# Kernel optimization log

Hardware: AMD Instinct MI355X
Metric: run time of the kernel (lower is better)

The kernel has to match this reference:

```python
import jax, jax.numpy as jnp
import numpy as np

B_, L_, D_, N_ = 2, 2048, 512, 64

def setup_inputs() -> dict:
    key = jax.random.key(0)
    ks = jax.random.split(key, 6)
    s = 1.0 / np.sqrt(D_)
    return {
        "x": jax.random.normal(ks[0], (B_, L_, D_), dtype=jnp.float32),
        "W1": jax.random.normal(ks[1], (D_, D_), dtype=jnp.float32) * s,
        "b1": jnp.zeros((D_,), dtype=jnp.float32),
        "W2": jax.random.normal(ks[2], (D_, N_), dtype=jnp.float32) * s,
        "b2": jnp.zeros((N_,), dtype=jnp.float32),
        "W3": jax.random.normal(ks[3], (D_, N_), dtype=jnp.float32) * s,
        "b3": jnp.zeros((N_,), dtype=jnp.float32),
        "A": jax.random.normal(ks[4], (D_, N_), dtype=jnp.float32) * (1.0 / np.sqrt(N_)),
    }

def reference(x, W1, b1, W2, b2, W3, b3, A):
    # Projections (faithful to fc2/fc3/fc1 in the torch module)
    B = x @ W2 + b2                                  # (b, l, n)
    C = x @ W3 + b3                                  # (b, l, n)
    delta = jax.nn.softplus(x @ W1 + b1)             # (b, l, d)
    # Discretization
    dB = jnp.einsum('bld,bln->bldn', delta, B)       # (b, l, d, n)
    dA = jnp.exp(jnp.einsum('bld,dn->bldn', delta, A))  # (b, l, d, n)
    # h is initialized to zeros in the original forward, so the dA*h term
    # contributes exactly zero; kept for faithfulness to the source math.
    h = dA * 0.0 + x[..., None] * dB                 # (b, l, d, n)
    y = jnp.einsum('bln,bldn->bld', C, h)            # (b, l, d)
    return y
```

## Files before the change

### kernel.cpp

```cpp
#include <hip/hip_runtime.h>
#include <math.h>

#define DDIM 512
#define MTOK 4096

typedef _Float16 f16;
typedef _Float16 f16x4 __attribute__((ext_vector_type(4)));
typedef _Float16 f16x8 __attribute__((ext_vector_type(8)));
typedef float f32x4 __attribute__((ext_vector_type(4)));

__device__ __forceinline__ float softplusf(float v) {
    return (v > 20.0f) ? v : log1pf(__expf(v));
}

__device__ __forceinline__ void async_load16(const void* g, void* l) {
    __builtin_amdgcn_global_load_lds(
        (const __attribute__((address_space(1))) void*)g,
        (__attribute__((address_space(3))) void*)l, 16, 0, 0);
}

__global__ __launch_bounds__(256) void prep_kernel(
    const float* __restrict__ x,  const float* __restrict__ W1,
    const float* __restrict__ W2, const float* __restrict__ W3,
    f16* __restrict__ xh, f16* __restrict__ w1t, f16* __restrict__ w23)
{
    __shared__ __align__(16) f16 lt[32][520];
    const int tid  = threadIdx.x;
    const int bid  = blockIdx.x;
    const int wv   = tid >> 6;
    const int lane = tid & 63;
    const int q    = lane >> 4;
    const int l15  = lane & 15;

    if (bid < 256) {
        const int mt  = bid;
        const int row = tid >> 4;
        const int cg  = tid & 15;
        const float* xr = x + (size_t)(mt * 16 + row) * DDIM;
#pragma unroll
        for (int i = 0; i < 8; ++i) {
            int col = cg * 4 + i * 64;
            float4 v = *(const float4*)(xr + col);
            f16x4 h = {(f16)v.x, (f16)v.y, (f16)v.z, (f16)v.w};
            *(f16x4*)&lt[row][col] = h;
        }
        __syncthreads();
#pragma unroll
        for (int j = 0; j < 4; ++j) {
            int kt = wv * 4 + j;
            f16x8 vv = *(const f16x8*)&lt[l15][kt * 32 + q * 8];
            *(f16x8*)(xh + (size_t)(mt * 16 + kt) * 512 + lane * 8) = vv;
        }
        return;
    }
    int wb = bid - 256;
    const float* src; int srcRS, col0; f16* dst;
    if (wb < 16)      { src = W1; srcRS = DDIM; col0 = wb * 32;
                        dst = w1t + (size_t)wb * 2 * 16 * 512; }
    else if (wb < 18) { src = W2; srcRS = 64;  col0 = (wb - 16) * 32;
                        dst = w23 + (size_t)(wb - 16) * 2 * 16 * 512; }
    else              { src = W3; srcRS = 64;  col0 = (wb - 18) * 32;
                        dst = w23 + (size_t)(4 + (wb - 18) * 2) * 16 * 512; }
#pragma unroll
    for (int i = 0; i < 16; ++i) {
        int f  = tid + 256 * i;
        int k  = f >> 3;
        int c4 = (f & 7) * 4;
        float4 v = *(const float4*)(src + (size_t)k * srcRS + col0 + c4);
        lt[c4 + 0][k] = (f16)v.x; lt[c4 + 1][k] = (f16)v.y;
        lt[c4 + 2][k] = (f16)v.z; lt[c4 + 3][k] = (f16)v.w;
    }
    __syncthreads();
#pragma unroll
    for (int j = 0; j < 8; ++j) {
        int s   = wv * 8 + j;
        int ntL = s >> 4;
        int kt  = s & 15;
        f16x8 vv = *(const f16x8*)&lt[ntL * 16 + l15][kt * 32 + q * 8];
        *(f16x8*)(dst + (size_t)(ntL * 16 + kt) * 512 + lane * 8) = vv;
    }
}

#define S_BUF 18432
__global__ __launch_bounds__(256) void s_kernel(
    const f16* __restrict__ xh, const f16* __restrict__ w23,
    const float* __restrict__ b2, const float* __restrict__ b3,
    float* __restrict__ s_out)
{
    __shared__ __align__(16) char smem[2 * S_BUF + 256];
    float* sred = (float*)(smem + 2 * S_BUF);

    const int tid  = threadIdx.x;
    const int wv   = tid >> 6;
    const int lane = tid & 63;
    const int q    = lane >> 4;
    const int l15  = lane & 15;
    const int mtG  = blockIdx.x;
    const int tb   = mtG * 16;

    f32x4 acc[2];
    acc[0] = (f32x4){0.f, 0.f, 0.f, 0.f};
    acc[1] = (f32x4){0.f, 0.f, 0.f, 0.f};

    auto issue = [&](int buf, int it) {
        int kt0 = it * 2;
#pragma unroll
        for (int j = 0; j < 5; ++j) {
            int id = wv + 4 * j;
            if (id >= 18) break;
            const f16* g; int off;
            if (id < 2) {
                g   = xh + (size_t)(mtG * 16 + kt0 + id) * 512 + lane * 8;
                off = id * 1024;
            } else {
                int t = id - 2, nt = t >> 1, kk = t & 1;
                g   = w23 + (size_t)(nt * 16 + kt0 + kk) * 512 + lane * 8;
                off = 2048 + t * 1024;
            }
            async_load16(g, smem + buf * S_BUF + off);
        }
    };

    issue(0, 0);
    for (int it = 0; it < 8; ++it) {
        __syncthreads();
        if (it + 1 < 8) issue((it + 1) & 1, it + 1);
        const char* xb = smem + (it & 1) * S_BUF;
        const char* wb = xb + 2048;
#pragma unroll
        for (int kk = 0; kk < 2; ++kk) {
            f16x8 a  = *(const f16x8*)(xb + kk * 1024 + lane * 16);
            f16x8 bB = *(const f16x8*)(wb + ((wv * 2 + kk)) * 1024 + lane * 16);
            f16x8 bC = *(const f16x8*)(wb + (((4 + wv) * 2 + kk)) * 1024 + lane * 16);
            acc[0] = __builtin_amdgcn_mfma_f32_16x16x32_f16(a, bB, acc[0], 0, 0, 0);
            acc[1] = __builtin_amdgcn_mfma_f32_16x16x32_f16(a, bC, acc[1], 0, 0, 0);
        }
    }

    float b2v = b2[wv * 16 + l15];
    float b3v = b3[wv * 16 + l15];
#pragma unroll
    for (int r = 0; r < 4; ++r) {
        float p = (acc[0][r] + b2v) * (acc[1][r] + b3v);
        p += __shfl_xor(p, 1); p += __shfl_xor(p, 2);
        p += __shfl_xor(p, 4); p += __shfl_xor(p, 8);
        if (l15 == 0) sred[wv * 16 + q * 4 + r] = p;
    }
    __syncthreads();
    if (tid < 16)
        s_out[tb + tid] = sred[tid] + sred[16 + tid] + sred[32 + tid] + sred[48 + tid];
}

#define Y_BUF 24576
__global__ __launch_bounds__(512) void y_kernel(
    const f16* __restrict__ xh, const f16* __restrict__ w1t,
    const float* __restrict__ x, const float* __restrict__ b1,
    const float* __restrict__ s_in, float* __restrict__ y)
{
    __shared__ __align__(16) char smem[2 * Y_BUF];

    const int tid  = threadIdx.x;
    const int wv   = tid >> 6;
    const int lane = tid & 63;
    const int q    = lane >> 4;
    const int l15  = lane & 15;
    const int db   = blockIdx.x * 64;
    const int ntG  = blockIdx.x * 4;
    const int tb   = blockIdx.y * 128;
    const int mtG  = blockIdx.y * 8;

    f32x4 acc[4];
#pragma unroll
    for (int nt = 0; nt < 4; ++nt) acc[nt] = (f32x4){0.f, 0.f, 0.f, 0.f};

    auto issue = [&](int buf, int it) {
        int kt0 = it * 2;
#pragma unroll
        for (int j = 0; j < 3; ++j) {
            int id = wv * 3 + j;
            const f16* g; int off;
            if (id < 16) {
                int mt = id >> 1, kk = id & 1;
                g   = xh + (size_t)((mtG + mt) * 16 + kt0 + kk) * 512 + lane * 8;
                off = id * 1024;
            } else {
                int t = id - 16, nt = t >> 1, kk = t & 1;
                g   = w1t + (size_t)((ntG + nt) * 16 + kt0 + kk) * 512 + lane * 8;
                off = 16384 + t * 1024;
            }
            async_load16(g, smem + buf * Y_BUF + off);
        }
    };

    issue(0, 0);
    for (int it = 0; it < 8; ++it) {
        __syncthreads();
        if (it + 1 < 8) issue((it + 1) & 1, it + 1);
        const char* xb = smem + (it & 1) * Y_BUF;
        const char* wb = xb + 16384;
#pragma unroll
        for (int kk = 0; kk < 2; ++kk) {
            f16x8 a = *(const f16x8*)(xb + (wv * 2 + kk) * 1024 + lane * 16);
#pragma unroll
            for (int nt = 0; nt < 4; ++nt) {
                f16x8 b = *(const f16x8*)(wb + (nt * 2 + kk) * 1024 + lane * 16);
                acc[nt] = __builtin_amdgcn_mfma_f32_16x16x32_f16(a, b, acc[nt], 0, 0, 0);
            }
        }
    }

    float b1v[4];
#pragma unroll
    for (int nt = 0; nt < 4; ++nt) b1v[nt] = b1[db + nt * 16 + l15];
#pragma unroll
    for (int r = 0; r < 4; ++r) {
        int token = tb + wv * 16 + q * 4 + r;
        float st = s_in[token];
#pragma unroll
        for (int nt = 0; nt < 4; ++nt) {
            int d = db + nt * 16 + l15;
            float xv = x[(size_t)token * DDIM + d];
            y[(size_t)token * DDIM + d] = xv * softplusf(acc[nt][r] + b1v[nt]) * st;
        }
    }
}

extern "C" void kernel_launch(void* const* d_in, const int* in_sizes, int n_in,
                              void* d_out, int out_size, void* d_ws, size_t ws_size,
                              hipStream_t stream)
{
    (void)n_in; (void)out_size; (void)ws_size; (void)in_sizes;
    const float* x  = (const float*)d_in[0];
    const float* W1 = (const float*)d_in[1];
    const float* b1 = (const float*)d_in[2];
    const float* W2 = (const float*)d_in[3];
    const float* b2 = (const float*)d_in[4];
    const float* W3 = (const float*)d_in[5];
    const float* b3 = (const float*)d_in[6];
    float* y = (float*)d_out;

    char* ws  = (char*)d_ws;
    f16* xh   = (f16*)(ws);
    f16* w1t  = (f16*)(ws + (4 << 20));
    f16* w23  = (f16*)(ws + (4 << 20) + (512 << 10));
    float* sv = (float*)(ws + (5 << 20));

    prep_kernel<<<276, 256, 0, stream>>>(x, W1, W2, W3, xh, w1t, w23);
    s_kernel<<<MTOK / 16, 256, 0, stream>>>(xh, w23, b2, b3, sv);
    y_kernel<<<dim3(DDIM / 64, MTOK / 128), 512, 0, stream>>>(xh, w1t, x, b1, sv, y);
}
```

Before: 97.60 us.

## Fuse x conversion into s_kernel and drop LDS staging in GEMM kernels

Moves the x fp32-to-fp16 conversion out of the prep kernel and into s_kernel, which converts its 16-token tile into LDS, writes the packed xh copy, and uses the LDS tile directly as the A operand. The double-buffered async global-to-LDS pipelines in s_kernel and y_kernel are replaced with direct per-lane global loads of pre-packed MFMA fragments. y_kernel is retiled to 64x64 blocks with 8 waves, each wave owning one 16-token row tile and two 16-column tiles, which doubles the grid size. This removes one pass over x and the LDS/barrier overhead, but loses operand sharing through LDS and depends on L2 for reuse of xh and W1 tiles.

```diff
diff --git a/kernel.cpp b/kernel.cpp
--- a/kernel.cpp
+++ b/kernel.cpp
@@ -2,7 +2,6 @@
 #include <math.h>
 
 #define DDIM 512
-#define MTOK 4096
 
 typedef _Float16 f16;
 typedef _Float16 f16x4 __attribute__((ext_vector_type(4)));
@@ -13,47 +12,18 @@
     return (v > 20.0f) ? v : log1pf(__expf(v));
 }
 
-__device__ __forceinline__ void async_load16(const void* g, void* l) {
-    __builtin_amdgcn_global_load_lds(
-        (const __attribute__((address_space(1))) void*)g,
-        (__attribute__((address_space(3))) void*)l, 16, 0, 0);
-}
-
-__global__ __launch_bounds__(256) void prep_kernel(
-    const float* __restrict__ x,  const float* __restrict__ W1,
-    const float* __restrict__ W2, const float* __restrict__ W3,
-    f16* __restrict__ xh, f16* __restrict__ w1t, f16* __restrict__ w23)
+__global__ __launch_bounds__(256) void prep_w(
+    const float* __restrict__ W1, const float* __restrict__ W2,
+    const float* __restrict__ W3, f16* __restrict__ w1t, f16* __restrict__ w23)
 {
     __shared__ __align__(16) f16 lt[32][520];
     const int tid  = threadIdx.x;
-    const int bid  = blockIdx.x;
+    const int wb   = blockIdx.x;
     const int wv   = tid >> 6;
     const int lane = tid & 63;
     const int q    = lane >> 4;
     const int l15  = lane & 15;
 
-    if (bid < 256) {
-        const int mt  = bid;
-        const int row = tid >> 4;
-        const int cg  = tid & 15;
-        const float* xr = x + (size_t)(mt * 16 + row) * DDIM;
-#pragma unroll
-        for (int i = 0; i < 8; ++i) {
-            int col = cg * 4 + i * 64;
-            float4 v = *(const float4*)(xr + col);
-            f16x4 h = {(f16)v.x, (f16)v.y, (f16)v.z, (f16)v.w};
-            *(f16x4*)&lt[row][col] = h;
-        }
-        __syncthreads();
-#pragma unroll
-        for (int j = 0; j < 4; ++j) {
-            int kt = wv * 4 + j;
-            f16x8 vv = *(const f16x8*)&lt[l15][kt * 32 + q * 8];
-            *(f16x8*)(xh + (size_t)(mt * 16 + kt) * 512 + lane * 8) = vv;
-        }
-        return;
-    }
-    int wb = bid - 256;
     const float* src; int srcRS, col0; f16* dst;
     if (wb < 16)      { src = W1; srcRS = DDIM; col0 = wb * 32;
                         dst = w1t + (size_t)wb * 2 * 16 * 512; }
@@ -81,14 +51,13 @@
     }
 }
 
-#define S_BUF 18432
 __global__ __launch_bounds__(256) void s_kernel(
-    const f16* __restrict__ xh, const f16* __restrict__ w23,
+    const float* __restrict__ x, const f16* __restrict__ w23,
     const float* __restrict__ b2, const float* __restrict__ b3,
-    float* __restrict__ s_out)
+    f16* __restrict__ xh, float* __restrict__ s_out)
 {
-    __shared__ __align__(16) char smem[2 * S_BUF + 256];
-    float* sred = (float*)(smem + 2 * S_BUF);
+    __shared__ __align__(16) f16 xs[16][520];
+    __shared__ float sred[64];
 
     const int tid  = threadIdx.x;
     const int wv   = tid >> 6;
@@ -98,50 +67,44 @@
     const int mtG  = blockIdx.x;
     const int tb   = mtG * 16;
 
-    f32x4 acc[2];
-    acc[0] = (f32x4){0.f, 0.f, 0.f, 0.f};
-    acc[1] = (f32x4){0.f, 0.f, 0.f, 0.f};
+    {
+        const int row = tid >> 4, cg = tid & 15;
+        const float* xr = x + (size_t)(tb + row) * DDIM;
+#pragma unroll
+        for (int i = 0; i < 8; ++i) {
+            int col = cg * 4 + i * 64;
+            float4 v = *(const float4*)(xr + col);
+            f16x4 h = {(f16)v.x, (f16)v.y, (f16)v.z, (f16)v.w};
+            *(f16x4*)&xs[row][col] = h;
+        }
+    }
+    __syncthreads();
 
-    auto issue = [&](int buf, int it) {
-        int kt0 = it * 2;
 #pragma unroll
-        for (int j = 0; j < 5; ++j) {
-            int id = wv + 4 * j;
-            if (id >= 18) break;
-            const f16* g; int off;
-            if (id < 2) {
-                g   = xh + (size_t)(mtG * 16 + kt0 + id) * 512 + lane * 8;
-                off = id * 1024;
-            } else {
-                int t = id - 2, nt = t >> 1, kk = t & 1;
-                g   = w23 + (size_t)(nt * 16 + kt0 + kk) * 512 + lane * 8;
-                off = 2048 + t * 1024;
-            }
-            async_load16(g, smem + buf * S_BUF + off);
-        }
-    };
+    for (int j = 0; j < 4; ++j) {
+        int kt = wv * 4 + j;
+        f16x8 vv = *(const f16x8*)&xs[l15][kt * 32 + q * 8];
+        *(f16x8*)(xh + (size_t)(mtG * 16 + kt) * 512 + lane * 8) = vv;
+    }
 
-    issue(0, 0);
-    for (int it = 0; it < 8; ++it) {
-        __syncthreads();
-        if (it + 1 < 8) issue((it + 1) & 1, it + 1);
-        const char* xb = smem + (it & 1) * S_BUF;
-        const char* wb = xb + 2048;
+    f32x4 acc0 = (f32x4){0.f, 0.f, 0.f, 0.f};
+    f32x4 acc1 = (f32x4){0.f, 0.f, 0.f, 0.f};
+    const f16* wB = w23 + (size_t)(wv    ) * 16 * 512 + lane * 8;
+    const f16* wC = w23 + (size_t)(wv + 4) * 16 * 512 + lane * 8;
 #pragma unroll
-        for (int kk = 0; kk < 2; ++kk) {
-            f16x8 a  = *(const f16x8*)(xb + kk * 1024 + lane * 16);
-            f16x8 bB = *(const f16x8*)(wb + ((wv * 2 + kk)) * 1024 + lane * 16);
-            f16x8 bC = *(const f16x8*)(wb + (((4 + wv) * 2 + kk)) * 1024 + lane * 16);
-            acc[0] = __builtin_amdgcn_mfma_f32_16x16x32_f16(a, bB, acc[0], 0, 0, 0);
-            acc[1] = __builtin_amdgcn_mfma_f32_16x16x32_f16(a, bC, acc[1], 0, 0, 0);
-        }
+    for (int kt = 0; kt < 16; ++kt) {
+        f16x8 a  = *(const f16x8*)&xs[l15][kt * 32 + q * 8];
+        f16x8 bB = *(const f16x8*)(wB + (size_t)kt * 512);
+        f16x8 bC = *(const f16x8*)(wC + (size_t)kt * 512);
+        acc0 = __builtin_amdgcn_mfma_f32_16x16x32_f16(a, bB, acc0, 0, 0, 0);
+        acc1 = __builtin_amdgcn_mfma_f32_16x16x32_f16(a, bC, acc1, 0, 0, 0);
     }
 
     float b2v = b2[wv * 16 + l15];
     float b3v = b3[wv * 16 + l15];
 #pragma unroll
     for (int r = 0; r < 4; ++r) {
-        float p = (acc[0][r] + b2v) * (acc[1][r] + b3v);
+        float p = (acc0[r] + b2v) * (acc1[r] + b3v);
         p += __shfl_xor(p, 1); p += __shfl_xor(p, 2);
         p += __shfl_xor(p, 4); p += __shfl_xor(p, 8);
         if (l15 == 0) sred[wv * 16 + q * 4 + r] = p;
@@ -151,77 +114,47 @@
         s_out[tb + tid] = sred[tid] + sred[16 + tid] + sred[32 + tid] + sred[48 + tid];
 }
 
-#define Y_BUF 24576
 __global__ __launch_bounds__(512) void y_kernel(
     const f16* __restrict__ xh, const f16* __restrict__ w1t,
     const float* __restrict__ x, const float* __restrict__ b1,
     const float* __restrict__ s_in, float* __restrict__ y)
 {
-    __shared__ __align__(16) char smem[2 * Y_BUF];
-
     const int tid  = threadIdx.x;
     const int wv   = tid >> 6;
     const int lane = tid & 63;
     const int q    = lane >> 4;
     const int l15  = lane & 15;
-    const int db   = blockIdx.x * 64;
-    const int ntG  = blockIdx.x * 4;
-    const int tb   = blockIdx.y * 128;
-    const int mtG  = blockIdx.y * 8;
+    const int mt   = wv & 3;
+    const int nh   = wv >> 2;
+    const int cB   = blockIdx.x;
+    const int rB   = blockIdx.y;
 
-    f32x4 acc[4];
+    const f16* aP  = xh  + (size_t)((rB * 4 + mt) * 16) * 512 + lane * 8;
+    const f16* bP0 = w1t + (size_t)((cB * 4 + nh * 2 + 0) * 16) * 512 + lane * 8;
+    const f16* bP1 = w1t + (size_t)((cB * 4 + nh * 2 + 1) * 16) * 512 + lane * 8;
+
+    f32x4 acc0 = (f32x4){0.f, 0.f, 0.f, 0.f};
+    f32x4 acc1 = (f32x4){0.f, 0.f, 0.f, 0.f};
 #pragma unroll
-    for (int nt = 0; nt < 4; ++nt) acc[nt] = (f32x4){0.f, 0.f, 0.f, 0.f};
-
-    auto issue = [&](int buf, int it) {
-        int kt0 = it * 2;
-#pragma unroll
-        for (int j = 0; j < 3; ++j) {
-            int id = wv * 3 + j;
-            const f16* g; int off;
-            if (id < 16) {
-                int mt = id >> 1, kk = id & 1;
-                g   = xh + (size_t)((mtG + mt) * 16 + kt0 + kk) * 512 + lane * 8;
-                off = id * 1024;
-            } else {
-                int t = id - 16, nt = t >> 1, kk = t & 1;
-                g   = w1t + (size_t)((ntG + nt) * 16 + kt0 + kk) * 512 + lane * 8;
-                off = 16384 + t * 1024;
-            }
-            async_load16(g, smem + buf * Y_BUF + off);
-        }
-    };
-
-    issue(0, 0);
-    for (int it = 0; it < 8; ++it) {
-        __syncthreads();
-        if (it + 1 < 8) issue((it + 1) & 1, it + 1);
-        const char* xb = smem + (it & 1) * Y_BUF;
-        const char* wb = xb + 16384;
-#pragma unroll
-        for (int kk = 0; kk < 2; ++kk) {
-            f16x8 a = *(const f16x8*)(xb + (wv * 2 + kk) * 1024 + lane * 16);
-#pragma unroll
-            for (int nt = 0; nt < 4; ++nt) {
-                f16x8 b = *(const f16x8*)(wb + (nt * 2 + kk) * 1024 + lane * 16);
-                acc[nt] = __builtin_amdgcn_mfma_f32_16x16x32_f16(a, b, acc[nt], 0, 0, 0);
-            }
-        }
+    for (int kt = 0; kt < 16; ++kt) {
+        f16x8 a  = *(const f16x8*)(aP  + (size_t)kt * 512);
+        f16x8 b0 = *(const f16x8*)(bP0 + (size_t)kt * 512);
+        f16x8 b1v = *(const f16x8*)(bP1 + (size_t)kt * 512);
+        acc0 = __builtin_amdgcn_mfma_f32_16x16x32_f16(a, b0,  acc0, 0, 0, 0);
+        acc1 = __builtin_amdgcn_mfma_f32_16x16x32_f16(a, b1v, acc1, 0, 0, 0);
     }
 
-    float b1v[4];
-#pragma unroll
-    for (int nt = 0; nt < 4; ++nt) b1v[nt] = b1[db + nt * 16 + l15];
+    const int d0 = cB * 64 + (nh * 2 + 0) * 16 + l15;
+    const int d1 = cB * 64 + (nh * 2 + 1) * 16 + l15;
+    const float bb0 = b1[d0], bb1 = b1[d1];
 #pragma unroll
     for (int r = 0; r < 4; ++r) {
-        int token = tb + wv * 16 + q * 4 + r;
+        int token = rB * 64 + mt * 16 + q * 4 + r;
         float st = s_in[token];
-#pragma unroll
-        for (int nt = 0; nt < 4; ++nt) {
-            int d = db + nt * 16 + l15;
-            float xv = x[(size_t)token * DDIM + d];
-            y[(size_t)token * DDIM + d] = xv * softplusf(acc[nt][r] + b1v[nt]) * st;
-        }
+        const float* xr = x + (size_t)token * DDIM;
+        float*       yr = y + (size_t)token * DDIM;
+        yr[d0] = xr[d0] * softplusf(acc0[r] + bb0) * st;
+        yr[d1] = xr[d1] * softplusf(acc1[r] + bb1) * st;
     }
 }
 
@@ -229,7 +162,7 @@
                               void* d_out, int out_size, void* d_ws, size_t ws_size,
                               hipStream_t stream)
 {
-    (void)n_in; (void)out_size; (void)ws_size; (void)in_sizes;
+    (void)n_in; (void)out_size; (void)ws_size;
     const float* x  = (const float*)d_in[0];
     const float* W1 = (const float*)d_in[1];
     const float* b1 = (const float*)d_in[2];
@@ -245,7 +178,9 @@
     f16* w23  = (f16*)(ws + (4 << 20) + (512 << 10));
     float* sv = (float*)(ws + (5 << 20));
 
-    prep_kernel<<<276, 256, 0, stream>>>(x, W1, W2, W3, xh, w1t, w23);
-    s_kernel<<<MTOK / 16, 256, 0, stream>>>(xh, w23, b2, b3, sv);
-    y_kernel<<<dim3(DDIM / 64, MTOK / 128), 512, 0, stream>>>(xh, w1t, x, b1, sv, y);
+    const int M = in_sizes[0] / DDIM;
+
+    prep_w<<<20, 256, 0, stream>>>(W1, W2, W3, w1t, w23);
+    s_kernel<<<M / 16, 256, 0, stream>>>(x, w23, b2, b3, xh, sv);
+    y_kernel<<<dim3(8, M / 64), 512, 0, stream>>>(xh, w1t, x, b1, sv, y);
 }
```

New measurement: 94.74 us (median of 2 runs). -2.9%, faster.
